# Optimization experiments

Hardware: AMD Instinct MI355X
Metric: run time of the kernel (lower is better)

## Reference

```python
import jax, jax.numpy as jnp
import numpy as np

N = 50000      # total nodes across all graphs
E = 1600000    # edges
G = 500        # graphs in batch
F = 128        # input node features
K = 5          # Chebyshev order


def setup_inputs() -> dict:
    key = jax.random.key(0)
    ks = jax.random.split(key, 12)
    x = jax.random.normal(ks[0], (N, F), dtype=jnp.float32)
    edge_index = jax.random.randint(ks[1], (2, E), 0, N)
    edge_attr = jax.random.uniform(ks[2], (E,), dtype=jnp.float32)
    batch = jnp.sort(jax.random.randint(ks[3], (N,), 0, G))
    s = 0.05
    W1 = jax.random.normal(ks[4], (K, F, 64), dtype=jnp.float32) * s
    b1 = jnp.zeros((64,), jnp.float32)
    W2 = jax.random.normal(ks[5], (K, 64, 64), dtype=jnp.float32) * s
    b2 = jnp.zeros((64,), jnp.float32)
    W3 = jax.random.normal(ks[6], (K, 64, 128), dtype=jnp.float32) * s
    b3 = jnp.zeros((128,), jnp.float32)
    Wl = jax.random.normal(ks[7], (128, 2), dtype=jnp.float32) * s
    bl = jnp.zeros((2,), jnp.float32)
    return {"x": x, "edge_index": edge_index, "edge_attr": edge_attr,
            "batch": batch, "W1": W1, "b1": b1, "W2": W2, "b2": b2,
            "W3": W3, "b3": b3, "Wl": Wl, "bl": bl}


def _cheb_conv(x, src, dst, w, Wk, b):
    """PyG ChebConv with lambda_max=2, sym norm: Lhat = -D^-1/2 A D^-1/2
    (the +I diag of L cancels the -I of the rescale, so only off-diag edges).
    Chebyshev recursion: Tx0=x, Tx1=Lhat x, Tx_k = 2 Lhat Tx_{k-1} - Tx_{k-2}."""
    n = x.shape[0]

    def prop(h):  # sparse matvec: out[i] = sum_{e: dst=i} w_e * h[src_e]
        return jax.ops.segment_sum(w[:, None] * h[src], dst, num_segments=n)

    Tx0 = x
    out = Tx0 @ Wk[0]
    Tx1 = prop(Tx0)
    out = out + Tx1 @ Wk[1]
    for k in range(2, Wk.shape[0]):
        Tx2 = 2.0 * prop(Tx1) - Tx0
        out = out + Tx2 @ Wk[k]
        Tx0, Tx1 = Tx1, Tx2
    return out + b


def reference(x, edge_index, edge_attr, batch, W1, b1, W2, b2, W3, b3, Wl, bl):
    src, dst = edge_index[0], edge_index[1]
    # sym-normalized scaled Laplacian edge weights (off-diagonal part)
    deg = jax.ops.segment_sum(edge_attr, src, num_segments=N)
    deg_safe = jnp.where(deg > 0, deg, 1.0)
    dinv = jnp.where(deg > 0, deg_safe ** -0.5, 0.0)
    w = -dinv[src] * edge_attr * dinv[dst]

    h = jax.nn.relu(_cheb_conv(x, src, dst, w, W1, b1))
    # dropout is identity at inference (training=False)
    h = jax.nn.relu(_cheb_conv(h, src, dst, w, W2, b2))
    h = jax.nn.relu(_cheb_conv(h, src, dst, w, W3, b3))

    # global_mean_pool over batch vector
    cnt = jax.ops.segment_sum(jnp.ones((N,), h.dtype), batch, num_segments=G)
    pooled = jax.ops.segment_sum(h, batch, num_segments=G) / jnp.maximum(cnt, 1.0)[:, None]

    logits = pooled @ Wl + bl
    return jax.nn.log_softmax(logits, axis=1)
```

## Files before the change

### kernel.cpp

```cpp
#include <hip/hip_runtime.h>
#include <hip/hip_bf16.h>

#define NN 50000
#define EE 1600000
#define GG 500

#define HB 6250
#define GX1 196
#define GB1 (GX1 * 5)
#define CVB 240

typedef __bf16 bf16x8 __attribute__((ext_vector_type(8)));
typedef float  f32x4  __attribute__((ext_vector_type(4)));

__device__ __forceinline__ float b2f(ushort u) {
  return __uint_as_float(((unsigned)u) << 16);
}
__device__ __forceinline__ ushort f2b(float f) {
  unsigned u = __float_as_uint(f);
  unsigned r = (u + 0x7fff + ((u >> 16) & 1)) >> 16;
  return (ushort)r;
}
__device__ __forceinline__ float lo16(uint v) { return __uint_as_float(v << 16); }
__device__ __forceinline__ float hi16(uint v) { return __uint_as_float(v & 0xffff0000u); }


__global__ __launch_bounds__(256) void mega1(
    const int* __restrict__ src, const int* __restrict__ dst,
    const float* __restrict__ ea, float* __restrict__ deg,
    int* __restrict__ cnt, int* __restrict__ rank,
    const float* __restrict__ x, const float* __restrict__ W1,
    ushort* __restrict__ Acat,
    const float* __restrict__ W2, const float* __restrict__ W3,
    ushort* __restrict__ Wt2, ushort* __restrict__ Wt3)
{
  int b = blockIdx.x;
  if (b < HB) {
    int i = b * 256 + threadIdx.x;
    if (i < EE) {
      atomicAdd(&deg[src[i]], ea[i]);
      rank[i] = atomicAdd(&cnt[dst[i]], 1);
    }
    return;
  }
  b -= HB;
  if (b < GB1) {
    const int bx = b % GX1, by = b / GX1;
    const int lane = threadIdx.x & 63;
    const int wid  = threadIdx.x >> 6;
    const int rb = bx * 256;
    const int cb = by * 64;
    const int lr = lane & 15;
    const int lk = (lane >> 4) << 3;
    f32x4 acc[4][4] = {};
    for (int kc = 0; kc < 128; kc += 64) {
      bf16x8 bfrag[2][4];
      #pragma unroll
      for (int ks = 0; ks < 2; ++ks)
        #pragma unroll
        for (int nt = 0; nt < 4; ++nt) {
          int col = cb + nt * 16 + lr;
          int kk  = kc + ks * 32 + lk;
          const float* wp = &W1[((size_t)(col >> 6) * 128 + kk) * 64 + (col & 63)];
          union { bf16x8 v; ushort u[8]; } bu;
          #pragma unroll
          for (int t = 0; t < 8; ++t) bu.u[t] = f2b(wp[t * 64]);
          bfrag[ks][nt] = bu.v;
        }
      #pragma unroll
      for (int s = 0; s < 4; ++s) {
        const int row = rb + (wid * 4 + s) * 16 + lr;
        #pragma unroll
        for (int ks = 0; ks < 2; ++ks) {
          union { bf16x8 v; ushort u[8]; } au;
          if (row < NN) {
            const float* ap = &x[(size_t)row * 128 + kc + ks * 32 + lk];
            float4 f0 = *(const float4*)ap;
            float4 f1 = *(const float4*)(ap + 4);
            au.u[0] = f2b(f0.x); au.u[1] = f2b(f0.y);
            au.u[2] = f2b(f0.z); au.u[3] = f2b(f0.w);
            au.u[4] = f2b(f1.x); au.u[5] = f2b(f1.y);
            au.u[6] = f2b(f1.z); au.u[7] = f2b(f1.w);
          } else {
            au.v = bf16x8{};
          }
          #pragma unroll
          for (int nt = 0; nt < 4; ++nt)
            acc[s][nt] = __builtin_amdgcn_mfma_f32_16x16x32_bf16(au.v, bfrag[ks][nt],
                                                                 acc[s][nt], 0, 0, 0);
        }
      }
    }
    #pragma unroll
    for (int s = 0; s < 4; ++s)
      #pragma unroll
      for (int nt = 0; nt < 4; ++nt) {
        const int col = cb + nt * 16 + lr;
        #pragma unroll
        for (int r = 0; r < 4; ++r) {
          const int row = rb + (wid * 4 + s) * 16 + ((lane >> 4) << 2) + r;
          if (row < NN) Acat[(size_t)row * 320 + col] = f2b(acc[s][nt][r]);
        }
      }
    return;
  }
  b -= GB1;
  int t = b * 256 + threadIdx.x;
  if (t < 320 * 64) {
    int j = t / 64, k = t % 64;
    Wt2[t] = f2b(W2[((size_t)(j >> 6) * 64 + k) * 64 + (j & 63)]);
  } else {
    int t2 = t - 320 * 64;
    int j = t2 / 320, k = t2 % 320;
    Wt3[t2] = f2b(W3[(size_t)k * 128 + j]);
  }
}


__global__ void scan1(const int* __restrict__ cnt, float* __restrict__ deg,
                      int* __restrict__ partial, int* __restrict__ bsum, int n) {
  __shared__ int s[256];
  int t = threadIdx.x, i = blockIdx.x * 256 + t;
  if (i < n) { float d = deg[i]; deg[i] = (d > 0.f) ? (1.0f / sqrtf(d)) : 0.f; }
  int v = (i < n) ? ((cnt[i] + 3) & ~3) : 0;
  s[t] = v; __syncthreads();
  for (int off = 1; off < 256; off <<= 1) {
    int xv = (t >= off) ? s[t - off] : 0;
    __syncthreads(); s[t] += xv; __syncthreads();
  }
  if (i < n) partial[i] = s[t];
  if (t == 255) bsum[blockIdx.x] = s[255];
}

__global__ void scan2(int* __restrict__ bsum, int nb) {
  __shared__ int s[256];
  int t = threadIdx.x;
  int v = (t < nb) ? bsum[t] : 0;
  s[t] = v; __syncthreads();
  for (int off = 1; off < 256; off <<= 1) {
    int xv = (t >= off) ? s[t - off] : 0;
    __syncthreads(); s[t] += xv; __syncthreads();
  }
  if (t < nb) bsum[t] = s[t];
}

__global__ void scan3(const int* __restrict__ partial, const int* __restrict__ bsum,
                      const int* __restrict__ cnt, int* __restrict__ rowptr,
                      uint2* __restrict__ edges, int n) {
  int i = blockIdx.x * 256 + threadIdx.x;
  if (i < n) {
    int off = (blockIdx.x > 0) ? bsum[blockIdx.x - 1] : 0;
    int end = partial[i] + off;
    rowptr[i + 1] = end;
    if (i == 0) rowptr[0] = 0;
    int c = cnt[i];
    int start = end - ((c + 3) & ~3);
    for (int q = start + c; q < end; ++q) edges[q] = make_uint2(0u, 0u);
  }
}

__global__ void scatter_kernel(const int* __restrict__ src, const int* __restrict__ dst,
                               const float* __restrict__ ea, const float* __restrict__ dinv,
                               const int* __restrict__ rowptr, const int* __restrict__ rank,
                               uint2* __restrict__ edges, int e) {
  int i = blockIdx.x * blockDim.x + threadIdx.x;
  if (i < e) {
    int s = src[i], d = dst[i];
    float w = -dinv[s] * ea[i] * dinv[d];
    edges[rowptr[d] + rank[i]] = make_uint2((unsigned)s, __float_as_uint(w));
  }
}


template<int NADD, bool RELUB>
__global__ __launch_bounds__(256) void prop_kernel(
    const int* __restrict__ rowptr, const uint2* __restrict__ edges,
    const ushort* __restrict__ g, int sg,
    const ushort* __restrict__ a1, int sa1, float c1,
    const ushort* __restrict__ a2, int sa2, float c2,
    const float* __restrict__ bias,
    ushort* __restrict__ out, int so, int n, float alpha)
{
  const int wave = threadIdx.x >> 6;
  const int lane = threadIdx.x & 63;
  const int q    = lane >> 4;
  const int grp  = (lane >> 3) & 1;
  const int sub  = lane & 7;
  const int nd = (blockIdx.x * 4 + wave) * 4 + q;
  const int e0 = rowptr[nd];
  const int e1 = rowptr[nd + 1];

  float ra[8] = {}, rb[8] = {};
  int j = e0 + grp;
  for (; j + 2 < e1; j += 4) {
    uint2 p0 = edges[j];
    uint2 p1 = edges[j + 2];
    uint4 v0 = *(const uint4*)&g[(size_t)p0.x * sg + sub * 8];
    uint4 v1 = *(const uint4*)&g[(size_t)p1.x * sg + sub * 8];
    float w0 = __uint_as_float(p0.y);
    float w1 = __uint_as_float(p1.y);
    ra[0] += w0 * lo16(v0.x); ra[1] += w0 * hi16(v0.x);
    ra[2] += w0 * lo16(v0.y); ra[3] += w0 * hi16(v0.y);
    ra[4] += w0 * lo16(v0.z); ra[5] += w0 * hi16(v0.z);
    ra[6] += w0 * lo16(v0.w); ra[7] += w0 * hi16(v0.w);
    rb[0] += w1 * lo16(v1.x); rb[1] += w1 * hi16(v1.x);
    rb[2] += w1 * lo16(v1.y); rb[3] += w1 * hi16(v1.y);
    rb[4] += w1 * lo16(v1.z); rb[5] += w1 * hi16(v1.z);
    rb[6] += w1 * lo16(v1.w); rb[7] += w1 * hi16(v1.w);
  }
  float r[8];
  #pragma unroll
  for (int e = 0; e < 8; ++e) {
    float t = ra[e] + rb[e];
    t += __shfl_xor(t, 8, 64);
    r[e] = alpha * t;
  }
  if constexpr (NADD >= 1) {
    uint4 u = *(const uint4*)&a1[(size_t)nd * sa1 + sub * 8];
    r[0] += c1 * lo16(u.x); r[1] += c1 * hi16(u.x);
    r[2] += c1 * lo16(u.y); r[3] += c1 * hi16(u.y);
    r[4] += c1 * lo16(u.z); r[5] += c1 * hi16(u.z);
    r[6] += c1 * lo16(u.w); r[7] += c1 * hi16(u.w);
  }
  if constexpr (NADD >= 2) {
    uint4 u = *(const uint4*)&a2[(size_t)nd * sa2 + sub * 8];
    r[0] += c2 * lo16(u.x); r[1] += c2 * hi16(u.x);
    r[2] += c2 * lo16(u.y); r[3] += c2 * hi16(u.y);
    r[4] += c2 * lo16(u.z); r[5] += c2 * hi16(u.z);
    r[6] += c2 * lo16(u.w); r[7] += c2 * hi16(u.w);
  }
  if constexpr (RELUB) {
    float4 b0 = *(const float4*)&bias[sub * 8];
    float4 b1 = *(const float4*)&bias[sub * 8 + 4];
    r[0] = fmaxf(r[0] + b0.x, 0.f); r[1] = fmaxf(r[1] + b0.y, 0.f);
    r[2] = fmaxf(r[2] + b0.z, 0.f); r[3] = fmaxf(r[3] + b0.w, 0.f);
    r[4] = fmaxf(r[4] + b1.x, 0.f); r[5] = fmaxf(r[5] + b1.y, 0.f);
    r[6] = fmaxf(r[6] + b1.z, 0.f); r[7] = fmaxf(r[7] + b1.w, 0.f);
  }
  if (grp == 0) {
    uint4 o;
    o.x = (uint)f2b(r[0]) | ((uint)f2b(r[1]) << 16);
    o.y = (uint)f2b(r[2]) | ((uint)f2b(r[3]) << 16);
    o.z = (uint)f2b(r[4]) | ((uint)f2b(r[5]) << 16);
    o.w = (uint)f2b(r[6]) | ((uint)f2b(r[7]) << 16);
    *(uint4*)&out[(size_t)nd * so + sub * 8] = o;
  }
}


template<int Ci, int Co, bool BR>
__global__ __launch_bounds__(256) void gemm_mfma(const ushort* __restrict__ A,
    const ushort* __restrict__ Wt, const float* __restrict__ bias,
    ushort* __restrict__ C, int n)
{
  const int lane = threadIdx.x & 63;
  const int wid  = threadIdx.x >> 6;
  const int rb = blockIdx.x * 256;
  const int cb = blockIdx.y * 64;
  const int lr = lane & 15;
  const int lk = (lane >> 4) << 3;
  f32x4 acc[4][4] = {};

  for (int kc = 0; kc < Ci; kc += 64) {
    bf16x8 bfrag[2][4];
    #pragma unroll
    for (int ks = 0; ks < 2; ++ks)
      #pragma unroll
      for (int nt = 0; nt < 4; ++nt)
        bfrag[ks][nt] = *(const bf16x8*)&Wt[(size_t)(cb + nt * 16 + lr) * Ci + kc + ks * 32 + lk];
    #pragma unroll
    for (int s = 0; s < 4; ++s) {
      const int row = rb + (wid * 4 + s) * 16 + lr;
      const ushort* ap = &A[(size_t)row * Ci + kc + lk];
      #pragma unroll
      for (int ks = 0; ks < 2; ++ks) {
        bf16x8 af = {};
        if (row < n) af = *(const bf16x8*)(ap + ks * 32);
        #pragma unroll
        for (int nt = 0; nt < 4; ++nt)
          acc[s][nt] = __builtin_amdgcn_mfma_f32_16x16x32_bf16(af, bfrag[ks][nt], acc[s][nt], 0, 0, 0);
      }
    }
  }

  #pragma unroll
  for (int s = 0; s < 4; ++s)
    #pragma unroll
    for (int nt = 0; nt < 4; ++nt) {
      const int col = cb + nt * 16 + lr;
      #pragma unroll
      for (int r = 0; r < 4; ++r) {
        const int row = rb + (wid * 4 + s) * 16 + ((lane >> 4) << 2) + r;
        if (row < n) {
          float v = acc[s][nt][r];
          if constexpr (BR) v = fmaxf(v + bias[col], 0.f);
          C[(size_t)row * Co + col] = f2b(v);
        }
      }
    }
}


__global__ __launch_bounds__(128) void pool_kernel(const ushort* __restrict__ h,
    const int* __restrict__ batch, float* __restrict__ pooled,
    float* __restrict__ gcnt, int n) {
  const int f = threadIdx.x;
  const int i0 = blockIdx.x * 64;
  const int iend = min(i0 + 64, n);
  int cur = batch[i0];
  float acc = 0.f;
  int run = 0;
  for (int i = i0; i < iend; ++i) {
    int b = batch[i];
    float v = b2f(h[(size_t)i * 128 + f]);
    if (b != cur) {
      atomicAdd(&pooled[cur * 128 + f], acc);
      if (f == 0) atomicAdd(&gcnt[cur], (float)run);
      acc = 0.f; run = 0; cur = b;
    }
    acc += v; run++;
  }
  atomicAdd(&pooled[cur * 128 + f], acc);
  if (f == 0) atomicAdd(&gcnt[cur], (float)run);
}

__global__ __launch_bounds__(128) void head_kernel(const float* __restrict__ pooled,
    const float* __restrict__ gcnt, const float* __restrict__ Wl,
    const float* __restrict__ bl, float* __restrict__ outp)
{
  int g = blockIdx.x, t = threadIdx.x;
  float denom = fmaxf(gcnt[g], 1.f);
  float p = pooled[g * 128 + t] / denom;
  __shared__ float s0[128], s1[128];
  s0[t] = p * Wl[t * 2 + 0];
  s1[t] = p * Wl[t * 2 + 1];
  __syncthreads();
  for (int off = 64; off > 0; off >>= 1) {
    if (t < off) { s0[t] += s0[t + off]; s1[t] += s1[t + off]; }
    __syncthreads();
  }
  if (t == 0) {
    float a = s0[0] + bl[0], b = s1[0] + bl[1];
    float m = fmaxf(a, b);
    float z = logf(expf(a - m) + expf(b - m)) + m;
    outp[g * 2 + 0] = a - z;
    outp[g * 2 + 1] = b - z;
  }
}


extern "C" void kernel_launch(void* const* d_in, const int* in_sizes, int n_in,
                              void* d_out, int out_size, void* d_ws, size_t ws_size,
                              hipStream_t stream) {
  const float* x   = (const float*)d_in[0];
  const int*   ei  = (const int*)d_in[1];
  const float* ea  = (const float*)d_in[2];
  const int* batch = (const int*)d_in[3];
  const float* W1  = (const float*)d_in[4];
  const float* lb1 = (const float*)d_in[5];
  const float* W2  = (const float*)d_in[6];
  const float* lb2 = (const float*)d_in[7];
  const float* W3  = (const float*)d_in[8];
  const float* lb3 = (const float*)d_in[9];
  const float* Wl  = (const float*)d_in[10];
  const float* bl  = (const float*)d_in[11];
  const int* srcv = ei;
  const int* dstv = ei + EE;

  char* w = (char*)d_ws;
  auto alloc = [&](size_t bytes) -> char* {
    char* p = w; w += (bytes + 255) & ~(size_t)255; return p;
  };
  float* deg    = (float*)alloc((size_t)NN * 4);
  int*   cnt    = (int*)alloc((size_t)NN * 4);
  float* pooled = (float*)alloc((size_t)(GG * 128 + GG) * 4);
  float* gcnt   = pooled + GG * 128;
  char*  zero_end = w;
  int*   rowptr = (int*)alloc((size_t)(NN + 1) * 4);
  int*   bsum   = (int*)alloc(256 * 4);
  int*   rank   = (int*)alloc((size_t)EE * 4);
  uint2* edges  = (uint2*)alloc((size_t)(EE + 4 * NN) * 8);
  ushort* Acat  = (ushort*)alloc((size_t)NN * 320 * 2);
  ushort* Bcat  = (ushort*)alloc((size_t)NN * 320 * 2);
  ushort* h1    = (ushort*)alloc((size_t)NN * 64 * 2);
  ushort* Wt2   = (ushort*)alloc((size_t)320 * 64 * 2);
  ushort* Wt3   = (ushort*)alloc((size_t)128 * 320 * 2);
  int*   partial = (int*)Bcat;
  ushort* h3 = Bcat;

  hipMemsetAsync(deg, 0, (size_t)(zero_end - (char*)deg), stream);

  mega1<<<HB + GB1 + CVB, 256, 0, stream>>>(srcv, dstv, ea, deg, cnt, rank,
                                            x, W1, Acat, W2, W3, Wt2, Wt3);

  const int nb = (NN + 255) / 256;
  scan1<<<nb, 256, 0, stream>>>(cnt, deg, partial, bsum, NN);
  scan2<<<1, 256, 0, stream>>>(bsum, nb);
  scan3<<<nb, 256, 0, stream>>>(partial, bsum, cnt, rowptr, edges, NN);
  scatter_kernel<<<(EE + 255) / 256, 256, 0, stream>>>(srcv, dstv, ea, deg, rowptr, rank,
                                                       edges, EE);

  const int PG = NN / 16;
  const int GX = (NN + 255) / 256;

  ushort* A0 = Acat + 0 * 64;  ushort* A1 = Acat + 1 * 64;  ushort* A2 = Acat + 2 * 64;
  ushort* A3 = Acat + 3 * 64;  ushort* A4 = Acat + 4 * 64;
  ushort* B0 = Bcat + 0 * 64;  ushort* B1 = Bcat + 1 * 64;  ushort* B2 = Bcat + 2 * 64;
  ushort* B3 = Bcat + 3 * 64;  ushort* B4 = Bcat + 4 * 64;
  const int S = 320;

  prop_kernel<1, false><<<PG, 256, 0, stream>>>(rowptr, edges, A4, S, A3, S, 1.f,
      nullptr, 0, 0.f, nullptr, A3, S, NN, 2.f);
  prop_kernel<2, false><<<PG, 256, 0, stream>>>(rowptr, edges, A3, S, A2, S, 1.f,
      A4, S, -1.f, nullptr, A2, S, NN, 2.f);
  prop_kernel<2, false><<<PG, 256, 0, stream>>>(rowptr, edges, A2, S, A1, S, 1.f,
      A3, S, -1.f, nullptr, A1, S, NN, 2.f);
  prop_kernel<2, true><<<PG, 256, 0, stream>>>(rowptr, edges, A1, S, A0, S, 1.f,
      A2, S, -1.f, lb1, h1, 64, NN, 1.f);

  gemm_mfma<64, 320, false><<<dim3(GX, 5), 256, 0, stream>>>(h1, Wt2, nullptr, Bcat, NN);
  prop_kernel<1, false><<<PG, 256, 0, stream>>>(rowptr, edges, B4, S, B3, S, 1.f,
      nullptr, 0, 0.f, nullptr, B3, S, NN, 2.f);
  prop_kernel<2, false><<<PG, 256, 0, stream>>>(rowptr, edges, B3, S, B2, S, 1.f,
      B4, S, -1.f, nullptr, B2, S, NN, 2.f);
  prop_kernel<2, false><<<PG, 256, 0, stream>>>(rowptr, edges, B2, S, B1, S, 1.f,
      B3, S, -1.f, nullptr, B1, S, NN, 2.f);
  prop_kernel<2, true><<<PG, 256, 0, stream>>>(rowptr, edges, B1, S, B0, S, 1.f,
      B2, S, -1.f, lb2, A0, S, NN, 1.f);

  prop_kernel<0, false><<<PG, 256, 0, stream>>>(rowptr, edges, A0, S, nullptr, 0, 0.f,
      nullptr, 0, 0.f, nullptr, A1, S, NN, 1.f);
  prop_kernel<1, false><<<PG, 256, 0, stream>>>(rowptr, edges, A1, S, A0, S, -1.f,
      nullptr, 0, 0.f, nullptr, A2, S, NN, 2.f);
  prop_kernel<1, false><<<PG, 256, 0, stream>>>(rowptr, edges, A2, S, A1, S, -1.f,
      nullptr, 0, 0.f, nullptr, A3, S, NN, 2.f);
  prop_kernel<1, false><<<PG, 256, 0, stream>>>(rowptr, edges, A3, S, A2, S, -1.f,
      nullptr, 0, 0.f, nullptr, A4, S, NN, 2.f);
  gemm_mfma<320, 128, true><<<dim3(GX, 2), 256, 0, stream>>>(Acat, Wt3, lb3, h3, NN);

  pool_kernel<<<(NN + 63) / 64, 128, 0, stream>>>(h3, batch, pooled, gcnt, NN);
  head_kernel<<<GG, 128, 0, stream>>>(pooled, gcnt, Wl, bl, (float*)d_out);
}
```

Measured before the change: 614.9 us.

## Split 64-wide feature planes into two 32-wide halves for propagation gathers

Stores each Chebyshev feature block as two planar 32-column halves instead of interleaving all blocks with a 320-column row stride. The propagation kernel now launches one block set per half, gathers 64-byte rows with 4 edges × 4 lanes per node, and reduces across lanes with an extra shuffle. The first-layer GEMM epilogue and both MFMA GEMMs are adapted to read or write the split layout. The intent is to shrink the per-kernel gather working set so it stays resident in cache, and to avoid wide-strided rows. The cost is twice as many blocks, each re-reading rowptr and edges, plus a tail path that assumes rows are padded to a multiple of 4 edges.

```diff
diff --git a/kernel.cpp b/kernel.cpp
--- a/kernel.cpp
+++ b/kernel.cpp
@@ -9,6 +9,7 @@
 #define GX1 196
 #define GB1 (GX1 * 5)
 #define CVB 240
+#define PHB (NN / 16)
 
 typedef __bf16 bf16x8 __attribute__((ext_vector_type(8)));
 typedef float  f32x4  __attribute__((ext_vector_type(4)));
@@ -23,6 +24,7 @@
 }
 __device__ __forceinline__ float lo16(uint v) { return __uint_as_float(v << 16); }
 __device__ __forceinline__ float hi16(uint v) { return __uint_as_float(v & 0xffff0000u); }
+
 
 
 __global__ __launch_bounds__(256) void mega1(
@@ -91,15 +93,17 @@
         }
       }
     }
+    const size_t kbase = (size_t)by * (NN * 64);
     #pragma unroll
     for (int s = 0; s < 4; ++s)
       #pragma unroll
       for (int nt = 0; nt < 4; ++nt) {
-        const int col = cb + nt * 16 + lr;
+        const int ci = nt * 16 + lr;
+        ushort* cp = Acat + kbase + (size_t)(ci >> 5) * (NN * 32) + (ci & 31);
         #pragma unroll
         for (int r = 0; r < 4; ++r) {
           const int row = rb + (wid * 4 + s) * 16 + ((lane >> 4) << 2) + r;
-          if (row < NN) Acat[(size_t)row * 320 + col] = f2b(acc[s][nt][r]);
+          if (row < NN) cp[(size_t)row * 32] = f2b(acc[s][nt][r]);
         }
       }
     return;
@@ -175,28 +179,32 @@
 template<int NADD, bool RELUB>
 __global__ __launch_bounds__(256) void prop_kernel(
     const int* __restrict__ rowptr, const uint2* __restrict__ edges,
-    const ushort* __restrict__ g, int sg,
-    const ushort* __restrict__ a1, int sa1, float c1,
-    const ushort* __restrict__ a2, int sa2, float c2,
+    const ushort* __restrict__ g,
+    const ushort* __restrict__ a1, float c1,
+    const ushort* __restrict__ a2, float c2,
     const float* __restrict__ bias,
-    ushort* __restrict__ out, int so, int n, float alpha)
+    ushort* __restrict__ out, float alpha)
 {
+  const int fh  = blockIdx.x / PHB;
+  const int blk = blockIdx.x % PHB;
   const int wave = threadIdx.x >> 6;
   const int lane = threadIdx.x & 63;
   const int q    = lane >> 4;
-  const int grp  = (lane >> 3) & 1;
-  const int sub  = lane & 7;
-  const int nd = (blockIdx.x * 4 + wave) * 4 + q;
+  const int e    = (lane >> 2) & 3;
+  const int sub  = lane & 3;
+  const int nd = (blk * 4 + wave) * 4 + q;
   const int e0 = rowptr[nd];
   const int e1 = rowptr[nd + 1];
+  const size_t hoff = (size_t)fh * (NN * 32);
+  const ushort* gh = g + hoff;
 
   float ra[8] = {}, rb[8] = {};
-  int j = e0 + grp;
-  for (; j + 2 < e1; j += 4) {
-    uint2 p0 = edges[j];
-    uint2 p1 = edges[j + 2];
-    uint4 v0 = *(const uint4*)&g[(size_t)p0.x * sg + sub * 8];
-    uint4 v1 = *(const uint4*)&g[(size_t)p1.x * sg + sub * 8];
+  int j = e0;
+  for (; j + 8 <= e1; j += 8) {
+    uint2 p0 = edges[j + e];
+    uint2 p1 = edges[j + 4 + e];
+    uint4 v0 = *(const uint4*)&gh[(size_t)p0.x * 32 + sub * 8];
+    uint4 v1 = *(const uint4*)&gh[(size_t)p1.x * 32 + sub * 8];
     float w0 = __uint_as_float(p0.y);
     float w1 = __uint_as_float(p1.y);
     ra[0] += w0 * lo16(v0.x); ra[1] += w0 * hi16(v0.x);
@@ -208,47 +216,58 @@
     rb[4] += w1 * lo16(v1.z); rb[5] += w1 * hi16(v1.z);
     rb[6] += w1 * lo16(v1.w); rb[7] += w1 * hi16(v1.w);
   }
+  if (j < e1) {
+    uint2 p = edges[j + e];
+    uint4 v = *(const uint4*)&gh[(size_t)p.x * 32 + sub * 8];
+    float w = __uint_as_float(p.y);
+    ra[0] += w * lo16(v.x); ra[1] += w * hi16(v.x);
+    ra[2] += w * lo16(v.y); ra[3] += w * hi16(v.y);
+    ra[4] += w * lo16(v.z); ra[5] += w * hi16(v.z);
+    ra[6] += w * lo16(v.w); ra[7] += w * hi16(v.w);
+  }
   float r[8];
   #pragma unroll
-  for (int e = 0; e < 8; ++e) {
-    float t = ra[e] + rb[e];
+  for (int k = 0; k < 8; ++k) {
+    float t = ra[k] + rb[k];
+    t += __shfl_xor(t, 4, 64);
     t += __shfl_xor(t, 8, 64);
-    r[e] = alpha * t;
+    r[k] = alpha * t;
   }
   if constexpr (NADD >= 1) {
-    uint4 u = *(const uint4*)&a1[(size_t)nd * sa1 + sub * 8];
+    uint4 u = *(const uint4*)&a1[hoff + (size_t)nd * 32 + sub * 8];
     r[0] += c1 * lo16(u.x); r[1] += c1 * hi16(u.x);
     r[2] += c1 * lo16(u.y); r[3] += c1 * hi16(u.y);
     r[4] += c1 * lo16(u.z); r[5] += c1 * hi16(u.z);
     r[6] += c1 * lo16(u.w); r[7] += c1 * hi16(u.w);
   }
   if constexpr (NADD >= 2) {
-    uint4 u = *(const uint4*)&a2[(size_t)nd * sa2 + sub * 8];
+    uint4 u = *(const uint4*)&a2[hoff + (size_t)nd * 32 + sub * 8];
     r[0] += c2 * lo16(u.x); r[1] += c2 * hi16(u.x);
     r[2] += c2 * lo16(u.y); r[3] += c2 * hi16(u.y);
     r[4] += c2 * lo16(u.z); r[5] += c2 * hi16(u.z);
     r[6] += c2 * lo16(u.w); r[7] += c2 * hi16(u.w);
   }
   if constexpr (RELUB) {
-    float4 b0 = *(const float4*)&bias[sub * 8];
-    float4 b1 = *(const float4*)&bias[sub * 8 + 4];
+    const float* bp = bias + fh * 32 + sub * 8;
+    float4 b0 = *(const float4*)bp;
+    float4 b1 = *(const float4*)(bp + 4);
     r[0] = fmaxf(r[0] + b0.x, 0.f); r[1] = fmaxf(r[1] + b0.y, 0.f);
     r[2] = fmaxf(r[2] + b0.z, 0.f); r[3] = fmaxf(r[3] + b0.w, 0.f);
     r[4] = fmaxf(r[4] + b1.x, 0.f); r[5] = fmaxf(r[5] + b1.y, 0.f);
     r[6] = fmaxf(r[6] + b1.z, 0.f); r[7] = fmaxf(r[7] + b1.w, 0.f);
   }
-  if (grp == 0) {
+  if (e == 0) {
     uint4 o;
     o.x = (uint)f2b(r[0]) | ((uint)f2b(r[1]) << 16);
     o.y = (uint)f2b(r[2]) | ((uint)f2b(r[3]) << 16);
     o.z = (uint)f2b(r[4]) | ((uint)f2b(r[5]) << 16);
     o.w = (uint)f2b(r[6]) | ((uint)f2b(r[7]) << 16);
-    *(uint4*)&out[(size_t)nd * so + sub * 8] = o;
-  }
-}
-
-
-template<int Ci, int Co, bool BR>
+    *(uint4*)&out[hoff + (size_t)nd * 32 + sub * 8] = o;
+  }
+}
+
+
+template<int Ci, int Co, bool SPLITA, bool SPLITC, bool BR>
 __global__ __launch_bounds__(256) void gemm_mfma(const ushort* __restrict__ A,
     const ushort* __restrict__ Wt, const float* __restrict__ bias,
     ushort* __restrict__ C, int n)
@@ -271,11 +290,18 @@
     #pragma unroll
     for (int s = 0; s < 4; ++s) {
       const int row = rb + (wid * 4 + s) * 16 + lr;
-      const ushort* ap = &A[(size_t)row * Ci + kc + lk];
       #pragma unroll
       for (int ks = 0; ks < 2; ++ks) {
         bf16x8 af = {};
-        if (row < n) af = *(const bf16x8*)(ap + ks * 32);
+        if (row < n) {
+          const ushort* ap;
+          if constexpr (SPLITA)
+            ap = A + (size_t)(kc >> 6) * ((size_t)n * 64) + (size_t)ks * ((size_t)n * 32)
+                   + (size_t)row * 32 + lk;
+          else
+            ap = A + (size_t)row * Ci + kc + ks * 32 + lk;
+          af = *(const bf16x8*)ap;
+        }
         #pragma unroll
         for (int nt = 0; nt < 4; ++nt)
           acc[s][nt] = __builtin_amdgcn_mfma_f32_16x16x32_bf16(af, bfrag[ks][nt], acc[s][nt], 0, 0, 0);
@@ -287,14 +313,19 @@
   for (int s = 0; s < 4; ++s)
     #pragma unroll
     for (int nt = 0; nt < 4; ++nt) {
-      const int col = cb + nt * 16 + lr;
+      const int ci = nt * 16 + lr;
+      const int col = cb + ci;
       #pragma unroll
       for (int r = 0; r < 4; ++r) {
         const int row = rb + (wid * 4 + s) * 16 + ((lane >> 4) << 2) + r;
         if (row < n) {
           float v = acc[s][nt][r];
           if constexpr (BR) v = fmaxf(v + bias[col], 0.f);
-          C[(size_t)row * Co + col] = f2b(v);
+          if constexpr (SPLITC)
+            C[(size_t)blockIdx.y * ((size_t)n * 64) + (size_t)(ci >> 5) * ((size_t)n * 32)
+              + (size_t)row * 32 + (ci & 31)] = f2b(v);
+          else
+            C[(size_t)row * Co + col] = f2b(v);
         }
       }
     }
@@ -400,43 +431,44 @@
   scatter_kernel<<<(EE + 255) / 256, 256, 0, stream>>>(srcv, dstv, ea, deg, rowptr, rank,
                                                        edges, EE);
 
-  const int PG = NN / 16;
+  const int PG = 2 * PHB;
   const int GX = (NN + 255) / 256;
 
-  ushort* A0 = Acat + 0 * 64;  ushort* A1 = Acat + 1 * 64;  ushort* A2 = Acat + 2 * 64;
-  ushort* A3 = Acat + 3 * 64;  ushort* A4 = Acat + 4 * 64;
-  ushort* B0 = Bcat + 0 * 64;  ushort* B1 = Bcat + 1 * 64;  ushort* B2 = Bcat + 2 * 64;
-  ushort* B3 = Bcat + 3 * 64;  ushort* B4 = Bcat + 4 * 64;
-  const int S = 320;
-
-  prop_kernel<1, false><<<PG, 256, 0, stream>>>(rowptr, edges, A4, S, A3, S, 1.f,
-      nullptr, 0, 0.f, nullptr, A3, S, NN, 2.f);
-  prop_kernel<2, false><<<PG, 256, 0, stream>>>(rowptr, edges, A3, S, A2, S, 1.f,
-      A4, S, -1.f, nullptr, A2, S, NN, 2.f);
-  prop_kernel<2, false><<<PG, 256, 0, stream>>>(rowptr, edges, A2, S, A1, S, 1.f,
-      A3, S, -1.f, nullptr, A1, S, NN, 2.f);
-  prop_kernel<2, true><<<PG, 256, 0, stream>>>(rowptr, edges, A1, S, A0, S, 1.f,
-      A2, S, -1.f, lb1, h1, 64, NN, 1.f);
-
-  gemm_mfma<64, 320, false><<<dim3(GX, 5), 256, 0, stream>>>(h1, Wt2, nullptr, Bcat, NN);
-  prop_kernel<1, false><<<PG, 256, 0, stream>>>(rowptr, edges, B4, S, B3, S, 1.f,
-      nullptr, 0, 0.f, nullptr, B3, S, NN, 2.f);
-  prop_kernel<2, false><<<PG, 256, 0, stream>>>(rowptr, edges, B3, S, B2, S, 1.f,
-      B4, S, -1.f, nullptr, B2, S, NN, 2.f);
-  prop_kernel<2, false><<<PG, 256, 0, stream>>>(rowptr, edges, B2, S, B1, S, 1.f,
-      B3, S, -1.f, nullptr, B1, S, NN, 2.f);
-  prop_kernel<2, true><<<PG, 256, 0, stream>>>(rowptr, edges, B1, S, B0, S, 1.f,
-      B2, S, -1.f, lb2, A0, S, NN, 1.f);
-
-  prop_kernel<0, false><<<PG, 256, 0, stream>>>(rowptr, edges, A0, S, nullptr, 0, 0.f,
-      nullptr, 0, 0.f, nullptr, A1, S, NN, 1.f);
-  prop_kernel<1, false><<<PG, 256, 0, stream>>>(rowptr, edges, A1, S, A0, S, -1.f,
-      nullptr, 0, 0.f, nullptr, A2, S, NN, 2.f);
-  prop_kernel<1, false><<<PG, 256, 0, stream>>>(rowptr, edges, A2, S, A1, S, -1.f,
-      nullptr, 0, 0.f, nullptr, A3, S, NN, 2.f);
-  prop_kernel<1, false><<<PG, 256, 0, stream>>>(rowptr, edges, A3, S, A2, S, -1.f,
-      nullptr, 0, 0.f, nullptr, A4, S, NN, 2.f);
-  gemm_mfma<320, 128, true><<<dim3(GX, 2), 256, 0, stream>>>(Acat, Wt3, lb3, h3, NN);
+  ushort* A0 = Acat + 0 * (size_t)NN * 64;  ushort* A1 = Acat + 1 * (size_t)NN * 64;
+  ushort* A2 = Acat + 2 * (size_t)NN * 64;  ushort* A3 = Acat + 3 * (size_t)NN * 64;
+  ushort* A4 = Acat + 4 * (size_t)NN * 64;
+  ushort* B0 = Bcat + 0 * (size_t)NN * 64;  ushort* B1 = Bcat + 1 * (size_t)NN * 64;
+  ushort* B2 = Bcat + 2 * (size_t)NN * 64;  ushort* B3 = Bcat + 3 * (size_t)NN * 64;
+  ushort* B4 = Bcat + 4 * (size_t)NN * 64;
+
+  prop_kernel<1, false><<<PG, 256, 0, stream>>>(rowptr, edges, A4, A3, 1.f,
+      nullptr, 0.f, nullptr, A3, 2.f);
+  prop_kernel<2, false><<<PG, 256, 0, stream>>>(rowptr, edges, A3, A2, 1.f,
+      A4, -1.f, nullptr, A2, 2.f);
+  prop_kernel<2, false><<<PG, 256, 0, stream>>>(rowptr, edges, A2, A1, 1.f,
+      A3, -1.f, nullptr, A1, 2.f);
+  prop_kernel<2, true><<<PG, 256, 0, stream>>>(rowptr, edges, A1, A0, 1.f,
+      A2, -1.f, lb1, h1, 1.f);
+
+  gemm_mfma<64, 320, true, true, false><<<dim3(GX, 5), 256, 0, stream>>>(h1, Wt2, nullptr, Bcat, NN);
+  prop_kernel<1, false><<<PG, 256, 0, stream>>>(rowptr, edges, B4, B3, 1.f,
+      nullptr, 0.f, nullptr, B3, 2.f);
+  prop_kernel<2, false><<<PG, 256, 0, stream>>>(rowptr, edges, B3, B2, 1.f,
+      B4, -1.f, nullptr, B2, 2.f);
+  prop_kernel<2, false><<<PG, 256, 0, stream>>>(rowptr, edges, B2, B1, 1.f,
+      B3, -1.f, nullptr, B1, 2.f);
+  prop_kernel<2, true><<<PG, 256, 0, stream>>>(rowptr, edges, B1, B0, 1.f,
+      B2, -1.f, lb2, A0, 1.f);
+
+  prop_kernel<0, false><<<PG, 256, 0, stream>>>(rowptr, edges, A0, nullptr, 0.f,
+      nullptr, 0.f, nullptr, A1, 1.f);
+  prop_kernel<1, false><<<PG, 256, 0, stream>>>(rowptr, edges, A1, A0, -1.f,
+      nullptr, 0.f, nullptr, A2, 2.f);
+  prop_kernel<1, false><<<PG, 256, 0, stream>>>(rowptr, edges, A2, A1, -1.f,
+      nullptr, 0.f, nullptr, A3, 2.f);
+  prop_kernel<1, false><<<PG, 256, 0, stream>>>(rowptr, edges, A3, A2, -1.f,
+      nullptr, 0.f, nullptr, A4, 2.f);
+  gemm_mfma<320, 128, true, false, true><<<dim3(GX, 2), 256, 0, stream>>>(Acat, Wt3, lb3, h3, NN);
 
   pool_kernel<<<(NN + 63) / 64, 128, 0, stream>>>(h3, batch, pooled, gcnt, NN);
   head_kernel<<<GG, 128, 0, stream>>>(pooled, gcnt, Wl, bl, (float*)d_out);
```

New measurement: 677.0 us. 10.1% more time.
